# Kernel optimization log

Measured on AMD Instinct MI355X. Metric: run time of the kernel, lower is better.

The kernel has to match this reference:

```python
import jax, jax.numpy as jnp
import numpy as np

D = 256

def setup_inputs() -> dict:
    key = jax.random.key(0)
    ks = iter(jax.random.split(key, 40))
    def nrm(shape, s=0.05):
        return (jax.random.normal(next(ks), shape, dtype=jnp.float32) * s)
    inp = {}
    inp['prot_data'] = jax.random.normal(next(ks), (8, 1000, 768), dtype=jnp.float32)
    inp['drug_data_ver'] = jax.random.normal(next(ks), (8, 56, 43), dtype=jnp.float32)
    inp['drug_data_adj'] = jax.random.uniform(next(ks), (8, 56, 56), dtype=jnp.float32)
    inp['prot_contacts'] = jax.random.uniform(next(ks), (8, 1000, 1000), dtype=jnp.float32)
    inp['prot_inter'] = jax.random.uniform(next(ks), (8, 1000, 56), dtype=jnp.float32)
    inp['prot_inter_exist'] = jax.random.uniform(next(ks), (8,), dtype=jnp.float32)
    inp['label'] = jax.random.normal(next(ks), (8, 1), dtype=jnp.float32)
    inp['fused_matrix'] = jax.random.normal(next(ks), (999, 1000), dtype=jnp.float32)
    # params
    inp['W_prot'] = nrm((768, D)); inp['b_prot'] = jnp.zeros((D,), jnp.float32)
    inp['gcn_W0'] = nrm((43, D));  inp['gcn_b0'] = jnp.zeros((D,), jnp.float32)
    inp['gcn_W1'] = nrm((D, D));   inp['gcn_b1'] = jnp.zeros((D,), jnp.float32)
    inp['gcn_W2'] = nrm((D, D));   inp['gcn_b2'] = jnp.zeros((D,), jnp.float32)
    inp['gcn_Wf'] = nrm((D, D));   inp['gcn_bf'] = jnp.zeros((D,), jnp.float32)
    inp['Wjp'] = nrm((D, D)); inp['bjp'] = jnp.zeros((D,), jnp.float32)
    inp['Wjc'] = nrm((D, D)); inp['bjc'] = jnp.zeros((D,), jnp.float32)
    inp['conv_w'] = nrm((64, 1, 4)); inp['conv_b'] = jnp.zeros((64,), jnp.float32)
    inp['W_r1'] = nrm((64 * 32, 600)); inp['b_r1'] = jnp.zeros((600,), jnp.float32)
    inp['W_r2'] = nrm((600, 300));     inp['b_r2'] = jnp.zeros((300,), jnp.float32)
    inp['W_r3'] = nrm((300, 1));       inp['b_r3'] = jnp.zeros((1,), jnp.float32)
    return inp

LAM_L1 = 1.0; LAM_FUSED = 1.0; LAM_GROUP = 1.0; LAM_BIND = 1.0

def reference(prot_data, drug_data_ver, drug_data_adj, prot_contacts, prot_inter,
              prot_inter_exist, label, fused_matrix,
              W_prot, b_prot, gcn_W0, gcn_b0, gcn_W1, gcn_b1, gcn_W2, gcn_b2,
              gcn_Wf, gcn_bf, Wjp, bjp, Wjc, bjc, conv_w, conv_b,
              W_r1, b_r1, W_r2, b_r2, W_r3, b_r3):
    # protein embedding (active path: single linear)
    prot = prot_data @ W_prot + b_prot                      # (b, 1000, 256)
    # compound GCN
    x = drug_data_ver
    for W, b in ((gcn_W0, gcn_b0), (gcn_W1, gcn_b1), (gcn_W2, gcn_b2)):
        x = jax.nn.relu(jnp.einsum('bij,bjd->bid', drug_data_adj, x @ W + b))
    comp = x @ gcn_Wf + gcn_bf                              # (b, 56, 256)
    # joint attention over prot x comp
    qp = jax.nn.relu(prot) @ Wjp + bjp
    qc = jax.nn.relu(comp) @ Wjc + bjc
    inter = jax.nn.sigmoid(jnp.einsum('bid,bkd->bik', qp, qc))  # (b, 1000, 56)
    inter = inter / jnp.sum(inter, axis=(1, 2), keepdims=True)
    # outer-product bilinear attention + weighted reduction (the 4D intermediate)
    cp4 = jnp.tanh(prot[:, :, None, :] * comp[:, None, :, :])   # (b, 1000, 56, 256)
    cp = jnp.einsum('bikd,bik->bd', cp4, inter)                 # (b, 256)
    h = cp[:, None, :]                                          # (b, 1, 256) NCH
    h = jax.lax.conv_general_dilated(h, conv_w, (2,), [(1, 1)],
                                     dimension_numbers=('NCH', 'OIH', 'NCH'))
    h = h + conv_b[None, :, None]                               # (b, 64, 128)
    h = jax.nn.leaky_relu(h, 0.1)
    h = jax.lax.reduce_window(h, -jnp.inf, jax.lax.max,
                              (1, 1, 4), (1, 1, 4), 'VALID')    # (b, 64, 32)
    h = h.reshape(h.shape[0], 64 * 32)
    h = jax.nn.leaky_relu(h @ W_r1 + b_r1, 0.1)
    h = jax.nn.leaky_relu(h @ W_r2 + b_r2, 0.1)
    affn = h @ W_r3 + b_r3                                      # (b, 1)
    # losses
    reg_l1 = jnp.mean(jnp.sum(jnp.abs(inter), axis=(1, 2)))
    reg_fused = jnp.mean(jnp.sum(jnp.abs(jnp.einsum('bij,ti->bjt', inter, fused_matrix)), axis=(1, 2)))
    group = jnp.sum(jnp.einsum('bij,bki->bjk', inter ** 2, prot_contacts), axis=1)  # (b, 1000)
    group = jnp.where(group == 0, group + 1e10, group)
    reg_group = jnp.mean(jnp.sum(jnp.sqrt(group) * jnp.sqrt(jnp.sum(prot_contacts, axis=2)), axis=1))
    loss0 = LAM_L1 * reg_l1 + LAM_FUSED * reg_fused + LAM_GROUP * reg_group
    lab_inter = prot_inter_exist[:, None, None] * prot_inter
    loss1 = jnp.mean(jnp.sqrt(jnp.sum((inter - lab_inter) ** 2, axis=(1, 2)))) * LAM_BIND
    loss2 = jnp.mean((affn - label) ** 2)
    return loss0 + loss1 + loss2
```

## Files before the change

kernel.cpp:

```cpp
#include <hip/hip_runtime.h>
#include <hip/hip_bf16.h>
#include <math.h>

#define B 8
#define NP 1000
#define NK 56
#define DP 768
#define DV 43
#define DD 256
#define NT 999

typedef __attribute__((ext_vector_type(8))) short bf16x8;
typedef __attribute__((ext_vector_type(4))) float f32x4;

__device__ inline short f2bf(float x) {
    __hip_bfloat16 h = __float2bfloat16(x);
    return __builtin_bit_cast(short, h);
}

template<bool RELU_IN>
__device__ __forceinline__ void gemm_body256(
    const float* __restrict__ A, const short* __restrict__ Wb,
    const float* __restrict__ bias, float* __restrict__ C,
    int K, int bm, int tid) {
    const int N = DD;
    int lane = tid & 63, w = tid >> 6;
    int m0 = bm * 32 + (w >> 1) * 16;
    int n0 = (w & 1) * 128;
    int lrow = lane & 15, lk = lane >> 4;
    f32x4 acc[8];
    #pragma unroll
    for (int nt = 0; nt < 8; ++nt) acc[nt] = {0.f, 0.f, 0.f, 0.f};
    const float* arow = A + (size_t)(m0 + lrow) * K + lk * 8;
    f32x4 a0 = *reinterpret_cast<const f32x4*>(arow);
    f32x4 a1 = *reinterpret_cast<const f32x4*>(arow + 4);
    for (int k0 = 0; k0 < K; k0 += 32) {
        f32x4 c0 = a0, c1 = a1;
        if (k0 + 32 < K) {
            a0 = *reinterpret_cast<const f32x4*>(arow + k0 + 32);
            a1 = *reinterpret_cast<const f32x4*>(arow + k0 + 36);
        }
        bf16x8 af;
        #pragma unroll
        for (int e = 0; e < 4; ++e) {
            float v0 = c0[e], v1 = c1[e];
            if (RELU_IN) { v0 = fmaxf(v0, 0.f); v1 = fmaxf(v1, 0.f); }
            af[e] = f2bf(v0); af[4 + e] = f2bf(v1);
        }
        const short* bbase = Wb + ((size_t)((k0 >> 3) + lk) * N + n0 + lrow) * 8;
        #pragma unroll
        for (int nt = 0; nt < 8; ++nt) {
            bf16x8 bf = *reinterpret_cast<const bf16x8*>(bbase + nt * 128);
            acc[nt] = __builtin_amdgcn_mfma_f32_16x16x32_bf16(af, bf, acc[nt], 0, 0, 0);
        }
    }
    #pragma unroll
    for (int nt = 0; nt < 8; ++nt) {
        int col = n0 + nt * 16 + lrow;
        float bv = bias[col];
        #pragma unroll
        for (int r = 0; r < 4; ++r) {
            int row = m0 + lk * 4 + r;
            C[(size_t)row * N + col] = acc[nt][r] + bv;
        }
    }
}

__device__ __forceinline__ void gcn_layer_body(
    const float* __restrict__ x, const float* __restrict__ adj,
    const float* __restrict__ W, const float* __restrict__ bias,
    float* __restrict__ y, int KIN, int bi, int tid,
    float* arow, float* u) {
    int b = bi / NK, i = bi % NK;
    if (tid < NK) arow[tid] = adj[((size_t)b * NK + i) * NK + tid];
    __syncthreads();
    if (tid < KIN) {
        float a0 = 0.f, a1 = 0.f;
        for (int j = 0; j < NK; j += 2) {
            a0 = fmaf(arow[j],     x[((size_t)b * NK + j)     * KIN + tid], a0);
            a1 = fmaf(arow[j + 1], x[((size_t)b * NK + j + 1) * KIN + tid], a1);
        }
        u[tid] = a0 + a1;
    }
    float rs = 0.f;
    for (int j = 0; j < NK; ++j) rs += arow[j];
    __syncthreads();
    float a0 = 0.f, a1 = 0.f, a2 = 0.f, a3 = 0.f;
    int kk = 0;
    for (; kk + 4 <= KIN; kk += 4) {
        a0 = fmaf(u[kk],     W[(size_t)kk * DD + tid],       a0);
        a1 = fmaf(u[kk + 1], W[(size_t)(kk + 1) * DD + tid], a1);
        a2 = fmaf(u[kk + 2], W[(size_t)(kk + 2) * DD + tid], a2);
        a3 = fmaf(u[kk + 3], W[(size_t)(kk + 3) * DD + tid], a3);
    }
    for (; kk < KIN; ++kk) a0 = fmaf(u[kk], W[(size_t)kk * DD + tid], a0);
    float v = a0 + a1 + a2 + a3 + rs * bias[tid];
    y[((size_t)b * NK + i) * DD + tid] = fmaxf(v, 0.f);
}

__device__ __forceinline__ void gcn_tail_body(
    const float* __restrict__ y1, const float* __restrict__ adj,
    const float* __restrict__ W2, const float* __restrict__ b2,
    const float* __restrict__ Wf, const float* __restrict__ bf,
    const float* __restrict__ Wjc, const float* __restrict__ bjc,
    float* __restrict__ comp, short* __restrict__ qcb,
    int bi, int tid, float* arow, float* u) {
    int b = bi / NK, i = bi % NK;
    if (tid < NK) arow[tid] = adj[((size_t)b * NK + i) * NK + tid];
    __syncthreads();
    {
        float a0 = 0.f, a1 = 0.f;
        for (int j = 0; j < NK; j += 2) {
            a0 = fmaf(arow[j],     y1[((size_t)b * NK + j)     * DD + tid], a0);
            a1 = fmaf(arow[j + 1], y1[((size_t)b * NK + j + 1) * DD + tid], a1);
        }
        u[tid] = a0 + a1;
    }
    float rs = 0.f;
    for (int j = 0; j < NK; ++j) rs += arow[j];
    __syncthreads();
    float a0 = 0.f, a1 = 0.f, a2 = 0.f, a3 = 0.f;
    #pragma unroll 4
    for (int kk = 0; kk < DD; kk += 4) {
        a0 = fmaf(u[kk],     W2[(size_t)kk * DD + tid],       a0);
        a1 = fmaf(u[kk + 1], W2[(size_t)(kk + 1) * DD + tid], a1);
        a2 = fmaf(u[kk + 2], W2[(size_t)(kk + 2) * DD + tid], a2);
        a3 = fmaf(u[kk + 3], W2[(size_t)(kk + 3) * DD + tid], a3);
    }
    float y2 = fmaxf(a0 + a1 + a2 + a3 + rs * b2[tid], 0.f);
    __syncthreads();
    u[tid] = y2;
    __syncthreads();
    a0 = a1 = a2 = a3 = 0.f;
    #pragma unroll 4
    for (int kk = 0; kk < DD; kk += 4) {
        a0 = fmaf(u[kk],     Wf[(size_t)kk * DD + tid],       a0);
        a1 = fmaf(u[kk + 1], Wf[(size_t)(kk + 1) * DD + tid], a1);
        a2 = fmaf(u[kk + 2], Wf[(size_t)(kk + 2) * DD + tid], a2);
        a3 = fmaf(u[kk + 3], Wf[(size_t)(kk + 3) * DD + tid], a3);
    }
    float cv = a0 + a1 + a2 + a3 + bf[tid];
    comp[((size_t)b * NK + i) * DD + tid] = cv;
    __syncthreads();
    u[tid] = fmaxf(cv, 0.f);
    __syncthreads();
    a0 = a1 = a2 = a3 = 0.f;
    #pragma unroll 4
    for (int kk = 0; kk < DD; kk += 4) {
        a0 = fmaf(u[kk],     Wjc[(size_t)kk * DD + tid],       a0);
        a1 = fmaf(u[kk + 1], Wjc[(size_t)(kk + 1) * DD + tid], a1);
        a2 = fmaf(u[kk + 2], Wjc[(size_t)(kk + 2) * DD + tid], a2);
        a3 = fmaf(u[kk + 3], Wjc[(size_t)(kk + 3) * DD + tid], a3);
    }
    float qv = a0 + a1 + a2 + a3 + bjc[tid];
    qcb[(((size_t)b * 32 + (tid >> 3)) * 64 + i) * 8 + (tid & 7)] = f2bf(qv);
}

__global__ __launch_bounds__(256) void k1_kernel(
    const float* __restrict__ W_prot, short* __restrict__ Wb1,
    const float* __restrict__ Wjp, short* __restrict__ Wb2,
    const float* __restrict__ fusedM, short* __restrict__ fMb,
    float* __restrict__ zero_region, float* __restrict__ qcb_zero,
    const float* __restrict__ drug_ver, const float* __restrict__ adj,
    const float* __restrict__ W0, const float* __restrict__ b0,
    float* __restrict__ y0) {
    __shared__ float smem[2112];
    int blk = blockIdx.x, tid = threadIdx.x;
    if (blk < 96) {
        int idx = blk * 256 + tid;
        int koct = idx / DD, n = idx % DD;
        bf16x8 v;
        #pragma unroll
        for (int e = 0; e < 8; ++e)
            v[e] = f2bf(W_prot[(size_t)(koct * 8 + e) * DD + n]);
        *reinterpret_cast<bf16x8*>(Wb1 + (size_t)idx * 8) = v;
    } else if (blk < 128) {
        int idx = (blk - 96) * 256 + tid;
        int koct = idx / DD, n = idx % DD;
        bf16x8 v;
        #pragma unroll
        for (int e = 0; e < 8; ++e)
            v[e] = f2bf(Wjp[(size_t)(koct * 8 + e) * DD + n]);
        *reinterpret_cast<bf16x8*>(Wb2 + (size_t)idx * 8) = v;
    } else if (blk < 640) {
        int blk2 = blk - 128;
        int t0 = (blk2 >> 3) * 16;
        int i0 = (blk2 & 7) * 128;
        for (int l = tid; l < 16 * 128; l += 256) {
            int tt = l >> 7, ii = l & 127;
            int t = t0 + tt, i = i0 + ii;
            smem[tt * 132 + ii] = (t < NT && i < NP) ? fusedM[(size_t)t * NP + i] : 0.f;
        }
        __syncthreads();
        int octl = tid >> 4, tl = tid & 15;
        bf16x8 v;
        #pragma unroll
        for (int e = 0; e < 8; ++e)
            v[e] = f2bf(smem[tl * 132 + octl * 8 + e]);
        size_t oct = i0 / 8 + octl;
        *reinterpret_cast<bf16x8*>(fMb + (oct * 1024 + t0 + tl) * 8) = v;
    } else if (blk < 677) {
        int idx = (blk - 640) * 256 + tid;
        if (idx < 48 + B * 600 + B * 300 + B * DD) zero_region[idx] = 0.f;
    } else if (blk < 933) {
        int idx = (blk - 677) * 256 + tid;
        qcb_zero[idx] = 0.f;
    } else {
        gcn_layer_body(drug_ver, adj, W0, b0, y0, DV, blk - 933, tid,
                       smem, smem + 64);
    }
}

__global__ __launch_bounds__(256) void k2_kernel(
    const float* __restrict__ prot_data, const short* __restrict__ Wb1,
    const float* __restrict__ b_prot, float* __restrict__ prot,
    const float* __restrict__ y0, const float* __restrict__ adj,
    const float* __restrict__ W1, const float* __restrict__ b1,
    float* __restrict__ y1) {
    __shared__ float smem[320];
    int blk = blockIdx.x, tid = threadIdx.x;
    if (blk < 250)
        gemm_body256<false>(prot_data, Wb1, b_prot, prot, DP, blk, tid);
    else
        gcn_layer_body(y0, adj, W1, b1, y1, DD, blk - 250, tid, smem, smem + 64);
}

__global__ __launch_bounds__(256) void k3_kernel(
    const float* __restrict__ prot, const short* __restrict__ Wb2,
    const float* __restrict__ bjp, float* __restrict__ qp,
    const float* __restrict__ y1, const float* __restrict__ adj,
    const float* __restrict__ W2, const float* __restrict__ b2,
    const float* __restrict__ Wf, const float* __restrict__ bf,
    const float* __restrict__ Wjc, const float* __restrict__ bjc,
    float* __restrict__ comp, short* __restrict__ qcb) {
    __shared__ float smem[320];
    int blk = blockIdx.x, tid = threadIdx.x;
    if (blk < 250)
        gemm_body256<true>(prot, Wb2, bjp, qp, DD, blk, tid);
    else
        gcn_tail_body(y1, adj, W2, b2, Wf, bf, Wjc, bjc, comp, qcb,
                      blk - 250, tid, smem, smem + 64);
}

__global__ __launch_bounds__(256) void inter_mfma_kernel(
    const float* __restrict__ qp, const short* __restrict__ qcb,
    const float* __restrict__ prot_inter, const float* __restrict__ exist,
    float* __restrict__ inter, float* __restrict__ s_bi,
    short* __restrict__ iTb, float* __restrict__ accums) {
    __shared__ float wred[4][4];
    int blk = blockIdx.x;
    int b = blk >> 4, mt = blk & 15;
    int tid = threadIdx.x;
    int lane = tid & 63, w = tid >> 6;
    int m0 = mt * 64 + w * 16;
    int lrow = lane & 15, lk = lane >> 4;
    f32x4 acc[4] = {{0.f,0.f,0.f,0.f},{0.f,0.f,0.f,0.f},
                    {0.f,0.f,0.f,0.f},{0.f,0.f,0.f,0.f}};
    int rowi = m0 + lrow;
    int rowc = (rowi < NP) ? rowi : (NP - 1);
    const float* arow = qp + ((size_t)b * NP + rowc) * DD + lk * 8;
    f32x4 a0 = *reinterpret_cast<const f32x4*>(arow);
    f32x4 a1 = *reinterpret_cast<const f32x4*>(arow + 4);
    for (int k0 = 0; k0 < DD; k0 += 32) {
        f32x4 c0 = a0, c1 = a1;
        if (k0 + 32 < DD) {
            a0 = *reinterpret_cast<const f32x4*>(arow + k0 + 32);
            a1 = *reinterpret_cast<const f32x4*>(arow + k0 + 36);
        }
        bf16x8 af;
        #pragma unroll
        for (int e = 0; e < 4; ++e) {
            af[e] = f2bf(c0[e]); af[4 + e] = f2bf(c1[e]);
        }
        const short* bb = qcb + (((size_t)b * 32 + (k0 >> 3) + lk) * 64 + lrow) * 8;
        #pragma unroll
        for (int nt = 0; nt < 4; ++nt) {
            bf16x8 bf = *reinterpret_cast<const bf16x8*>(bb + nt * 128);
            acc[nt] = __builtin_amdgcn_mfma_f32_16x16x32_bf16(af, bf, acc[nt], 0, 0, 0);
        }
    }
    float ex = exist[b];
    float aV = 0.f, aA = 0.f, aC = 0.f, aD = 0.f;
    float rowsq[4] = {0.f, 0.f, 0.f, 0.f};
    #pragma unroll
    for (int nt = 0; nt < 4; ++nt) {
        int j = nt * 16 + lrow;
        bool jv = (j < NK);
        #pragma unroll
        for (int r = 0; r < 4; ++r) {
            int i = m0 + lk * 4 + r;
            bool iv = (i < NP);
            float v = 0.f, lab = 0.f;
            if (jv) {
                if (iv) {
                    v = 1.f / (1.f + __expf(-acc[nt][r]));
                    lab = ex * prot_inter[((size_t)b * NP + i) * NK + j];
                    inter[((size_t)b * NP + i) * NK + j] = v;
                }
                iTb[(((size_t)(i >> 3) * 448 + b * NK + j) << 3) + (i & 7)] = f2bf(v);
            }
            aV += v; aA += v * v; aC += v * lab; aD += lab * lab;
            rowsq[r] += v * v;
        }
    }
    #pragma unroll
    for (int r = 0; r < 4; ++r) {
        float rs = rowsq[r];
        rs += __shfl_xor(rs, 1); rs += __shfl_xor(rs, 2);
        rs += __shfl_xor(rs, 4); rs += __shfl_xor(rs, 8);
        int i = m0 + lk * 4 + r;
        if (lrow == 0 && i < NP) s_bi[(size_t)b * NP + i] = rs;
    }
    #pragma unroll
    for (int off = 32; off; off >>= 1) {
        aV += __shfl_down(aV, off);
        aA += __shfl_down(aA, off);
        aC += __shfl_down(aC, off);
        aD += __shfl_down(aD, off);
    }
    if (lane == 0) {
        wred[w][0] = aV; wred[w][1] = aA; wred[w][2] = aC; wred[w][3] = aD;
    }
    __syncthreads();
    if (tid < 4) {
        float s = wred[0][tid] + wred[1][tid] + wred[2][tid] + wred[3][tid];
        atomicAdd(&accums[tid * 8 + b], s);
    }
}

__global__ __launch_bounds__(256) void k5_kernel(
    const float* __restrict__ prot, const float* __restrict__ comp,
    const float* __restrict__ inter, float* __restrict__ cp,
    const short* __restrict__ iTb, const short* __restrict__ fMb,
    float* __restrict__ fusedAbs,
    const float* __restrict__ contacts, const float* __restrict__ s_bi,
    const float* __restrict__ accums, float* __restrict__ groupv) {
    __shared__ float irow[8][NK];
    __shared__ float sb[8];
    int blk = blockIdx.x, tid = threadIdx.x;
    if (blk < 1000) {
        int b = blk / 125, chunk = blk % 125;
        int d = tid;
        float creg[NK];
        #pragma unroll
        for (int k = 0; k < NK; ++k)
            creg[k] = comp[((size_t)b * NK + k) * DD + d];
        for (int l = tid; l < 8 * NK; l += 256) {
            int ii = l / NK, k = l % NK;
            irow[ii][k] = inter[((size_t)b * NP + chunk * 8 + ii) * NK + k];
        }
        const float C2LOG2E = 2.8853900817779268f;
        float p2l[8];
        #pragma unroll
        for (int ii = 0; ii < 8; ++ii)
            p2l[ii] = C2LOG2E * prot[((size_t)b * NP + chunk * 8 + ii) * DD + d];
        __syncthreads();
        float acc0 = 0.f, acc1 = 0.f;
        #pragma unroll 1
        for (int ii = 0; ii < 8; ++ii) {
            float p = p2l[ii];
            #pragma unroll
            for (int k = 0; k < NK; k += 2) {
                float e0 = __builtin_amdgcn_exp2f(p * creg[k]);
                float e1 = __builtin_amdgcn_exp2f(p * creg[k + 1]);
                float r0 = __builtin_amdgcn_rcpf(e0 + 1.f);
                float r1 = __builtin_amdgcn_rcpf(e1 + 1.f);
                acc0 = fmaf(fmaf(-2.f, r0, 1.f), irow[ii][k],     acc0);
                acc1 = fmaf(fmaf(-2.f, r1, 1.f), irow[ii][k + 1], acc1);
            }
        }
        atomicAdd(&cp[(size_t)b * DD + d], acc0 + acc1);
    } else if (blk < 1112) {
        int fblk = blk - 1000;
        int mb = fblk % 14, nb = fblk / 14;
        int lane = tid & 63, w = tid >> 6;
        if (tid < 8) sb[tid] = 0.f;
        __syncthreads();
        int m0 = mb * 32 + (w >> 1) * 16;
        int n0 = nb * 128 + (w & 1) * 64;
        int lrow = lane & 15, lk = lane >> 4;
        f32x4 acc[4] = {{0.f,0.f,0.f,0.f},{0.f,0.f,0.f,0.f},
                        {0.f,0.f,0.f,0.f},{0.f,0.f,0.f,0.f}};
        for (int koct0 = 0; koct0 < 128; koct0 += 4) {
            int koct = koct0 + lk;
            bf16x8 af = *reinterpret_cast<const bf16x8*>(
                iTb + ((size_t)koct * 448 + m0 + lrow) * 8);
            const short* bb = fMb + ((size_t)koct * 1024 + n0 + lrow) * 8;
            #pragma unroll
            for (int nt = 0; nt < 4; ++nt) {
                bf16x8 bf = *reinterpret_cast<const bf16x8*>(bb + nt * 128);
                acc[nt] = __builtin_amdgcn_mfma_f32_16x16x32_bf16(af, bf, acc[nt], 0, 0, 0);
            }
        }
        #pragma unroll
        for (int r = 0; r < 4; ++r) {
            float part = fabsf(acc[0][r]) + fabsf(acc[1][r]) +
                         fabsf(acc[2][r]) + fabsf(acc[3][r]);
            #pragma unroll
            for (int off = 1; off < 16; off <<= 1)
                part += __shfl_xor(part, off);
            if (lrow == 0) {
                int row = m0 + lk * 4 + r;
                atomicAdd(&sb[row / NK], part);
            }
        }
        __syncthreads();
        if (tid < 8 && sb[tid] != 0.f) atomicAdd(&fusedAbs[tid], sb[tid]);
    } else {
        int w = tid >> 6, lane = tid & 63;
        int gk = (blk - 1112) * 4 + w;
        int b = gk / NP;
        const f32x4* row4 = reinterpret_cast<const f32x4*>(
            contacts + (size_t)gk * NP);
        const f32x4* sv4 = reinterpret_cast<const f32x4*>(s_bi + (size_t)b * NP);
        f32x4 z = {0.f, 0.f, 0.f, 0.f};
        f32x4 c0 = row4[lane];
        f32x4 c1 = row4[lane + 64];
        f32x4 c2 = row4[lane + 128];
        f32x4 c3 = z, s3 = z;
        f32x4 s0 = sv4[lane];
        f32x4 s1 = sv4[lane + 64];
        f32x4 s2 = sv4[lane + 128];
        if (lane + 192 < 250) { c3 = row4[lane + 192]; s3 = sv4[lane + 192]; }
        float g0 = 0.f, g1 = 0.f, g2 = 0.f, g3 = 0.f;
        #pragma unroll
        for (int e = 0; e < 4; ++e) {
            g0 = fmaf(c0[e], s0[e], g0);
            g1 = fmaf(c1[e], s1[e], g1);
            g2 = fmaf(c2[e], s2[e], g2);
            g3 = fmaf(c3[e], s3[e], g3);
        }
        float r0 = (c0[0] + c0[1]) + (c0[2] + c0[3]);
        float r1 = (c1[0] + c1[1]) + (c1[2] + c1[3]);
        float r2 = (c2[0] + c2[1]) + (c2[2] + c2[3]);
        float r3 = (c3[0] + c3[1]) + (c3[2] + c3[3]);
        float g = (g0 + g1) + (g2 + g3);
        float rs = (r0 + r1) + (r2 + r3);
        #pragma unroll
        for (int off = 32; off; off >>= 1) {
            g += __shfl_down(g, off);
            rs += __shfl_down(rs, off);
        }
        if (lane == 0) {
            float val;
            if (g == 0.f) val = sqrtf(1e10f) * sqrtf(rs);
            else          val = sqrtf(g) / accums[b] * sqrtf(rs);
            groupv[gk] = val;
        }
    }
}

__global__ __launch_bounds__(256) void fc1_conv_kernel(
    const float* __restrict__ cp, const float* __restrict__ accums,
    const float* __restrict__ conv_w, const float* __restrict__ conv_b,
    const float* __restrict__ W, float* __restrict__ raw) {
    const int N = 600, kchunk = 128;
    int t = threadIdx.x;
    int ol = t & 63;
    int o = blockIdx.x * 64 + ol;
    int w = t >> 6;
    int kbeg = blockIdx.y * kchunk;
    __shared__ float xS[B][258];
    __shared__ float sin_[B][128];
    for (int l = t; l < B * DD; l += 256) {
        int b = l >> 8, d = l & 255;
        xS[b][d + 1] = cp[(size_t)b * DD + d] / accums[b];
    }
    if (t < B) { xS[t][0] = 0.f; xS[t][257] = 0.f; }
    __syncthreads();
    for (int l = t; l < B * kchunk; l += 256) {
        int b = l >> 7, kl = l & 127;
        int kg = kbeg + kl;
        int oo = kg >> 5, p = kg & 31;
        float w0 = conv_w[oo * 4 + 0], w1 = conv_w[oo * 4 + 1];
        float w2 = conv_w[oo * 4 + 2], w3 = conv_w[oo * 4 + 3];
        float cb = conv_b[oo];
        float m = -INFINITY;
        #pragma unroll
        for (int q = 0; q < 4; ++q) {
            int base = (p * 4 + q) * 2;
            float acc = cb;
            acc = fmaf(xS[b][base + 0], w0, acc);
            acc = fmaf(xS[b][base + 1], w1, acc);
            acc = fmaf(xS[b][base + 2], w2, acc);
            acc = fmaf(xS[b][base + 3], w3, acc);
            acc = (acc > 0.f) ? acc : 0.1f * acc;
            m = fmaxf(m, acc);
        }
        sin_[b][kl] = m;
    }
    __syncthreads();
    float acc[B];
    #pragma unroll
    for (int b = 0; b < B; ++b) acc[b] = 0.f;
    for (int k = kbeg + w; k < kbeg + kchunk; k += 4) {
        float wv = W[(size_t)k * N + o];
        int kl = k - kbeg;
        #pragma unroll
        for (int b = 0; b < B; ++b)
            acc[b] = fmaf(sin_[b][kl], wv, acc[b]);
    }
    __shared__ float red[4][64][B];
    #pragma unroll
    for (int b = 0; b < B; ++b) red[w][ol][b] = acc[b];
    __syncthreads();
    for (int p = t; p < 64 * B; p += 256) {
        int oo = p / B, b = p % B;
        int o2 = blockIdx.x * 64 + oo;
        float s = red[0][oo][b] + red[1][oo][b] + red[2][oo][b] + red[3][oo][b];
        atomicAdd(&raw[(size_t)b * N + o2], s);
    }
}

__global__ __launch_bounds__(256) void fc2_kernel(
    const float* __restrict__ raw1, const float* __restrict__ b_r1,
    const float* __restrict__ W, float* __restrict__ raw2) {
    const int K = 600, N = 300, kchunk = 75;
    int t = threadIdx.x;
    int ol = t & 63;
    int o = blockIdx.x * 64 + ol;
    int w = t >> 6;
    int kbeg = blockIdx.y * kchunk;
    __shared__ float sin_[B][128];
    for (int l = t; l < B * kchunk; l += 256) {
        int b = l / kchunk, k = l % kchunk;
        float v = raw1[(size_t)b * K + kbeg + k] + b_r1[kbeg + k];
        v = (v > 0.f) ? v : 0.1f * v;
        sin_[b][k] = v;
    }
    __syncthreads();
    float acc[B];
    #pragma unroll
    for (int b = 0; b < B; ++b) acc[b] = 0.f;
    if (o < N) {
        for (int k = kbeg + w; k < kbeg + kchunk; k += 4) {
            float wv = W[(size_t)k * N + o];
            int kl = k - kbeg;
            #pragma unroll
            for (int b = 0; b < B; ++b)
                acc[b] = fmaf(sin_[b][kl], wv, acc[b]);
        }
    }
    __shared__ float red[4][64][B];
    #pragma unroll
    for (int b = 0; b < B; ++b) red[w][ol][b] = acc[b];
    __syncthreads();
    for (int p = t; p < 64 * B; p += 256) {
        int oo = p / B, b = p % B;
        int o2 = blockIdx.x * 64 + oo;
        if (o2 < N) {
            float s = red[0][oo][b] + red[1][oo][b] + red[2][oo][b] + red[3][oo][b];
            atomicAdd(&raw2[(size_t)b * N + o2], s);
        }
    }
}

__global__ __launch_bounds__(256) void final_kernel(
    const float* __restrict__ accums, const float* __restrict__ groupv,
    const float* __restrict__ raw2, const float* __restrict__ b_r2,
    const float* __restrict__ W3, const float* __restrict__ b3,
    const float* __restrict__ label, float* __restrict__ out) {
    int tid = threadIdx.x;
    __shared__ float affnS[8];
    {
        int b = tid >> 5, k0 = tid & 31;
        float acc = 0.f;
        for (int k = k0; k < 300; k += 32) {
            float v = raw2[(size_t)b * 300 + k] + b_r2[k];
            v = (v > 0.f) ? v : 0.1f * v;
            acc = fmaf(v, W3[k], acc);
        }
        #pragma unroll
        for (int off = 16; off; off >>= 1) acc += __shfl_down(acc, off);
        if (k0 == 0) affnS[b] = acc + b3[0];
    }
    float s = 0.f;
    for (int l = tid; l < B * NP; l += 256) s += groupv[l];
    __shared__ float r[256];
    r[tid] = s;
    __syncthreads();
    for (int st = 128; st; st >>= 1) {
        if (tid < st) r[tid] += r[tid + st];
        __syncthreads();
    }
    if (tid == 0) {
        float gtot = r[0];
        float l0 = 0.f, l1 = 0.f, l2 = 0.f;
        for (int b = 0; b < B; ++b) {
            float S = accums[b];
            float A = accums[8 + b], C = accums[16 + b], D = accums[24 + b];
            float fA = accums[32 + b];
            l0 += 1.f + fA / S;
            float bind = A / (S * S) - 2.f * C / S + D;
            l1 += sqrtf(fmaxf(bind, 0.f));
            float dd = affnS[b] - label[b];
            l2 += dd * dd;
        }
        out[0] = (l0 + gtot + l1 + l2) * 0.125f;
    }
}

extern "C" void kernel_launch(void* const* d_in, const int* in_sizes, int n_in,
                              void* d_out, int out_size, void* d_ws, size_t ws_size,
                              hipStream_t stream) {
    const float* prot_data   = (const float*)d_in[0];
    const float* drug_ver    = (const float*)d_in[1];
    const float* drug_adj    = (const float*)d_in[2];
    const float* contacts    = (const float*)d_in[3];
    const float* prot_inter  = (const float*)d_in[4];
    const float* exist       = (const float*)d_in[5];
    const float* label       = (const float*)d_in[6];
    const float* fused       = (const float*)d_in[7];
    const float* W_prot      = (const float*)d_in[8];
    const float* b_prot      = (const float*)d_in[9];
    const float* gcn_W0      = (const float*)d_in[10];
    const float* gcn_b0      = (const float*)d_in[11];
    const float* gcn_W1      = (const float*)d_in[12];
    const float* gcn_b1      = (const float*)d_in[13];
    const float* gcn_W2      = (const float*)d_in[14];
    const float* gcn_b2      = (const float*)d_in[15];
    const float* gcn_Wf      = (const float*)d_in[16];
    const float* gcn_bf      = (const float*)d_in[17];
    const float* Wjp         = (const float*)d_in[18];
    const float* bjp         = (const float*)d_in[19];
    const float* Wjc         = (const float*)d_in[20];
    const float* bjc         = (const float*)d_in[21];
    const float* conv_w      = (const float*)d_in[22];
    const float* conv_b      = (const float*)d_in[23];
    const float* W_r1        = (const float*)d_in[24];
    const float* b_r1        = (const float*)d_in[25];
    const float* W_r2        = (const float*)d_in[26];
    const float* b_r2        = (const float*)d_in[27];
    const float* W_r3        = (const float*)d_in[28];
    const float* b_r3        = (const float*)d_in[29];

    float* ws = (float*)d_ws;
    size_t off = 0;
    auto alloc = [&](size_t n) { float* p = ws + off; off += n; return p; };
    float* prot     = alloc((size_t)B * NP * DD);
    float* qp       = alloc((size_t)B * NP * DD);
    float* tbuf     = alloc((size_t)B * NK * DD);
    float* ybuf     = alloc((size_t)B * NK * DD);
    float* comp     = alloc((size_t)B * NK * DD);
    float* qcbF     = alloc((size_t)65536);
    float* inter    = alloc((size_t)B * NP * NK);
    float* s_bi     = alloc((size_t)B * NP);
    float* groupv   = alloc((size_t)B * NP);
    short* Wb1      = (short*)alloc((DP / 8) * DD * 8 / 2);
    short* Wb2      = (short*)alloc((DD / 8) * DD * 8 / 2);
    short* fMb      = (short*)alloc((size_t)128 * 1024 * 8 / 2);
    float* accums   = alloc(48);
    float* raw1     = alloc((size_t)B * 600);
    float* raw2     = alloc((size_t)B * 300);
    float* cp       = alloc((size_t)B * DD);

    short* qcb = (short*)qcbF;
    short* iTb = (short*)tbuf;
    (void)ybuf;

    k1_kernel<<<1381, 256, 0, stream>>>(W_prot, Wb1, Wjp, Wb2, fused, fMb,
                                        accums, qcbF, drug_ver, drug_adj,
                                        gcn_W0, gcn_b0, tbuf);

    k2_kernel<<<698, 256, 0, stream>>>(prot_data, Wb1, b_prot, prot,
                                       tbuf, drug_adj, gcn_W1, gcn_b1, ybuf);

    k3_kernel<<<698, 256, 0, stream>>>(prot, Wb2, bjp, qp,
                                       ybuf, drug_adj, gcn_W2, gcn_b2,
                                       gcn_Wf, gcn_bf, Wjc, bjc, comp, qcb);

    inter_mfma_kernel<<<128, 256, 0, stream>>>(
        qp, qcb, prot_inter, exist, inter, s_bi, iTb, accums);

    k5_kernel<<<3112, 256, 0, stream>>>(prot, comp, inter, cp,
                                        iTb, fMb, accums + 32,
                                        contacts, s_bi, accums, groupv);

    fc1_conv_kernel<<<dim3(10, 16), 256, 0, stream>>>(
        cp, accums, conv_w, conv_b, W_r1, raw1);

    fc2_kernel<<<dim3(5, 8), 256, 0, stream>>>(raw1, b_r1, W_r2, raw2);

    final_kernel<<<1, 256, 0, stream>>>(accums, groupv, raw2, b_r2,
                                        W_r3, b_r3, label, (float*)d_out);
}
```

Measured before the change: 137.7 us.

## Move group-norm contact rows from k5 into a merged fc1/conv kernel

The contacts group reduction blocks move out of the k5 kernel and merge with the fc1/conv kernel into a new k6 launch. This shortens k5 and lets the bandwidth-heavy contacts streaming overlap the small fc1 work instead of sitting beside the exp-heavy cp computation. The launch count stays the same. k6's fc1 blocks now carry the contacts blocks alongside them, which could change load balance.

```diff
diff --git a/kernel.cpp b/kernel.cpp
--- a/kernel.cpp
+++ b/kernel.cpp
@@ -332,9 +332,7 @@
     const float* __restrict__ prot, const float* __restrict__ comp,
     const float* __restrict__ inter, float* __restrict__ cp,
     const short* __restrict__ iTb, const short* __restrict__ fMb,
-    float* __restrict__ fusedAbs,
-    const float* __restrict__ contacts, const float* __restrict__ s_bi,
-    const float* __restrict__ accums, float* __restrict__ groupv) {
+    float* __restrict__ fusedAbs) {
     __shared__ float irow[8][NK];
     __shared__ float sb[8];
     int blk = blockIdx.x, tid = threadIdx.x;
@@ -370,7 +368,7 @@
             }
         }
         atomicAdd(&cp[(size_t)b * DD + d], acc0 + acc1);
-    } else if (blk < 1112) {
+    } else {
         int fblk = blk - 1000;
         int mb = fblk % 14, nb = fblk / 14;
         int lane = tid & 63, w = tid >> 6;
@@ -406,9 +404,76 @@
         }
         __syncthreads();
         if (tid < 8 && sb[tid] != 0.f) atomicAdd(&fusedAbs[tid], sb[tid]);
+    }
+}
+
+__global__ __launch_bounds__(256) void k6_kernel(
+    const float* __restrict__ cp, const float* __restrict__ accums,
+    const float* __restrict__ conv_w, const float* __restrict__ conv_b,
+    const float* __restrict__ W, float* __restrict__ raw,
+    const float* __restrict__ contacts, const float* __restrict__ s_bi,
+    float* __restrict__ groupv) {
+    int blk = blockIdx.x, t = threadIdx.x;
+    if (blk < 160) {
+        const int N = 600, kchunk = 128;
+        int ot = blk / 16, ks = blk % 16;
+        int ol = t & 63;
+        int o = ot * 64 + ol;
+        int w = t >> 6;
+        int kbeg = ks * kchunk;
+        __shared__ float xS[B][258];
+        __shared__ float sin_[B][128];
+        for (int l = t; l < B * DD; l += 256) {
+            int b = l >> 8, d = l & 255;
+            xS[b][d + 1] = cp[(size_t)b * DD + d] / accums[b];
+        }
+        if (t < B) { xS[t][0] = 0.f; xS[t][257] = 0.f; }
+        __syncthreads();
+        for (int l = t; l < B * kchunk; l += 256) {
+            int b = l >> 7, kl = l & 127;
+            int kg = kbeg + kl;
+            int oo = kg >> 5, p = kg & 31;
+            float w0 = conv_w[oo * 4 + 0], w1 = conv_w[oo * 4 + 1];
+            float w2 = conv_w[oo * 4 + 2], w3 = conv_w[oo * 4 + 3];
+            float cb = conv_b[oo];
+            float m = -INFINITY;
+            #pragma unroll
+            for (int q = 0; q < 4; ++q) {
+                int base = (p * 4 + q) * 2;
+                float acc = cb;
+                acc = fmaf(xS[b][base + 0], w0, acc);
+                acc = fmaf(xS[b][base + 1], w1, acc);
+                acc = fmaf(xS[b][base + 2], w2, acc);
+                acc = fmaf(xS[b][base + 3], w3, acc);
+                acc = (acc > 0.f) ? acc : 0.1f * acc;
+                m = fmaxf(m, acc);
+            }
+            sin_[b][kl] = m;
+        }
+        __syncthreads();
+        float acc[B];
+        #pragma unroll
+        for (int b = 0; b < B; ++b) acc[b] = 0.f;
+        for (int k = kbeg + w; k < kbeg + kchunk; k += 4) {
+            float wv = W[(size_t)k * N + o];
+            int kl = k - kbeg;
+            #pragma unroll
+            for (int b = 0; b < B; ++b)
+                acc[b] = fmaf(sin_[b][kl], wv, acc[b]);
+        }
+        __shared__ float red[4][64][B];
+        #pragma unroll
+        for (int b = 0; b < B; ++b) red[w][ol][b] = acc[b];
+        __syncthreads();
+        for (int p = t; p < 64 * B; p += 256) {
+            int oo = p / B, b = p % B;
+            int o2 = ot * 64 + oo;
+            float s = red[0][oo][b] + red[1][oo][b] + red[2][oo][b] + red[3][oo][b];
+            atomicAdd(&raw[(size_t)b * N + o2], s);
+        }
     } else {
-        int w = tid >> 6, lane = tid & 63;
-        int gk = (blk - 1112) * 4 + w;
+        int w = t >> 6, lane = t & 63;
+        int gk = (blk - 160) * 4 + w;
         int b = gk / NP;
         const f32x4* row4 = reinterpret_cast<const f32x4*>(
             contacts + (size_t)gk * NP);
@@ -447,68 +512,6 @@
             else          val = sqrtf(g) / accums[b] * sqrtf(rs);
             groupv[gk] = val;
         }
-    }
-}
-
-__global__ __launch_bounds__(256) void fc1_conv_kernel(
-    const float* __restrict__ cp, const float* __restrict__ accums,
-    const float* __restrict__ conv_w, const float* __restrict__ conv_b,
-    const float* __restrict__ W, float* __restrict__ raw) {
-    const int N = 600, kchunk = 128;
-    int t = threadIdx.x;
-    int ol = t & 63;
-    int o = blockIdx.x * 64 + ol;
-    int w = t >> 6;
-    int kbeg = blockIdx.y * kchunk;
-    __shared__ float xS[B][258];
-    __shared__ float sin_[B][128];
-    for (int l = t; l < B * DD; l += 256) {
-        int b = l >> 8, d = l & 255;
-        xS[b][d + 1] = cp[(size_t)b * DD + d] / accums[b];
-    }
-    if (t < B) { xS[t][0] = 0.f; xS[t][257] = 0.f; }
-    __syncthreads();
-    for (int l = t; l < B * kchunk; l += 256) {
-        int b = l >> 7, kl = l & 127;
-        int kg = kbeg + kl;
-        int oo = kg >> 5, p = kg & 31;
-        float w0 = conv_w[oo * 4 + 0], w1 = conv_w[oo * 4 + 1];
-        float w2 = conv_w[oo * 4 + 2], w3 = conv_w[oo * 4 + 3];
-        float cb = conv_b[oo];
-        float m = -INFINITY;
-        #pragma unroll
-        for (int q = 0; q < 4; ++q) {
-            int base = (p * 4 + q) * 2;
-            float acc = cb;
-            acc = fmaf(xS[b][base + 0], w0, acc);
-            acc = fmaf(xS[b][base + 1], w1, acc);
-            acc = fmaf(xS[b][base + 2], w2, acc);
-            acc = fmaf(xS[b][base + 3], w3, acc);
-            acc = (acc > 0.f) ? acc : 0.1f * acc;
-            m = fmaxf(m, acc);
-        }
-        sin_[b][kl] = m;
-    }
-    __syncthreads();
-    float acc[B];
-    #pragma unroll
-    for (int b = 0; b < B; ++b) acc[b] = 0.f;
-    for (int k = kbeg + w; k < kbeg + kchunk; k += 4) {
-        float wv = W[(size_t)k * N + o];
-        int kl = k - kbeg;
-        #pragma unroll
-        for (int b = 0; b < B; ++b)
-            acc[b] = fmaf(sin_[b][kl], wv, acc[b]);
-    }
-    __shared__ float red[4][64][B];
-    #pragma unroll
-    for (int b = 0; b < B; ++b) red[w][ol][b] = acc[b];
-    __syncthreads();
-    for (int p = t; p < 64 * B; p += 256) {
-        int oo = p / B, b = p % B;
-        int o2 = blockIdx.x * 64 + oo;
-        float s = red[0][oo][b] + red[1][oo][b] + red[2][oo][b] + red[3][oo][b];
-        atomicAdd(&raw[(size_t)b * N + o2], s);
     }
 }
 
@@ -672,12 +675,11 @@
     inter_mfma_kernel<<<128, 256, 0, stream>>>(
         qp, qcb, prot_inter, exist, inter, s_bi, iTb, accums);
 
-    k5_kernel<<<3112, 256, 0, stream>>>(prot, comp, inter, cp,
-                                        iTb, fMb, accums + 32,
-                                        contacts, s_bi, accums, groupv);
-
-    fc1_conv_kernel<<<dim3(10, 16), 256, 0, stream>>>(
-        cp, accums, conv_w, conv_b, W_r1, raw1);
+    k5_kernel<<<1112, 256, 0, stream>>>(prot, comp, inter, cp,
+                                        iTb, fMb, accums + 32);
+
+    k6_kernel<<<2160, 256, 0, stream>>>(cp, accums, conv_w, conv_b, W_r1, raw1,
+                                        contacts, s_bi, groupv);
 
     fc2_kernel<<<dim3(5, 8), 256, 0, stream>>>(raw1, b_r1, W_r2, raw2);
 
```

After: 140.0 us. Within noise of the previous version (+1.7%).
